# Kernel optimization log

Hardware: AMD Instinct MI355X
Metric: run time of the kernel (lower is better)

## Reference

```python
import jax, jax.numpy as jnp
import numpy as np

D_MODEL = 256
N_HEADS = 8
N_LEVELS = 4
NUM_POINTS_LIST = [4, 4, 4, 4]
SUM_POINTS = sum(NUM_POINTS_LIST)
TOTAL_POINTS = N_HEADS * SUM_POINTS
HEAD_DIM = D_MODEL // N_HEADS
OFFSET_SCALE = 0.5
SPATIAL_SHAPES = np.array([[80, 80], [40, 40], [20, 20], [10, 10]], dtype=np.int64)


def setup_inputs() -> dict:
    key = jax.random.key(0)
    ks = jax.random.split(key, 7)
    B, NQ = 16, 300
    seq = int((SPATIAL_SHAPES[:, 0] * SPATIAL_SHAPES[:, 1]).sum())  # 8500
    s = 1.0 / np.sqrt(D_MODEL)
    return {
        'hidden_states': jax.random.normal(ks[0], (B, NQ, D_MODEL), jnp.float32),
        'encoder_hidden_states': jax.random.normal(ks[1], (B, seq, D_MODEL), jnp.float32),
        'reference_points': jax.random.uniform(ks[2], (B, NQ, 1, 4), jnp.float32, 0.05, 0.95),
        'spatial_shapes': SPATIAL_SHAPES,
        'w_off': jax.random.uniform(ks[3], (TOTAL_POINTS * 2, D_MODEL), jnp.float32, -s, s),
        'b_off': jax.random.uniform(ks[4], (TOTAL_POINTS * 2,), jnp.float32, -s, s),
        'w_attn': jax.random.uniform(ks[5], (TOTAL_POINTS, D_MODEL), jnp.float32, -s, s),
        'b_attn': jax.random.uniform(ks[6], (TOTAL_POINTS,), jnp.float32, -s, s),
    }


def _grid_sample_zeros(img_flat, H, W, gx, gy):
    # img_flat: [N, H*W, C]; gx, gy: [N, Q, P] unnormalized pixel coords.
    # Bilinear, padding_mode='zeros', align_corners=False semantics of torch.grid_sample.
    x0 = jnp.floor(gx)
    y0 = jnp.floor(gy)
    wx = (gx - x0)[..., None]
    wy = (gy - y0)[..., None]
    x0i = x0.astype(jnp.int32)
    y0i = y0.astype(jnp.int32)

    def gather(xi, yi):
        valid = (xi >= 0) & (xi < W) & (yi >= 0) & (yi < H)
        idx = jnp.clip(yi, 0, H - 1) * W + jnp.clip(xi, 0, W - 1)
        N = img_flat.shape[0]
        v = jnp.take_along_axis(img_flat, idx.reshape(N, -1)[..., None], axis=1)
        v = v.reshape(idx.shape + (img_flat.shape[-1],))
        return v * valid[..., None]

    v00 = gather(x0i, y0i)
    v01 = gather(x0i + 1, y0i)
    v10 = gather(x0i, y0i + 1)
    v11 = gather(x0i + 1, y0i + 1)
    top = v00 * (1 - wx) + v01 * wx
    bot = v10 * (1 - wx) + v11 * wx
    return top * (1 - wy) + bot * wy  # [N, Q, P, C]


def reference(hidden_states, encoder_hidden_states, reference_points, spatial_shapes, w_off, b_off, w_attn, b_attn):
    B, NQ, _ = hidden_states.shape
    seq = encoder_hidden_states.shape[1]
    shapes = np.asarray(spatial_shapes)

    value = encoder_hidden_states.reshape(B, seq, N_HEADS, HEAD_DIM)

    off = (hidden_states @ w_off.T + b_off).reshape(B, NQ, N_HEADS, SUM_POINTS, 2)
    attn = jax.nn.softmax((hidden_states @ w_attn.T + b_attn).reshape(B, NQ, N_HEADS, SUM_POINTS), axis=-1)

    # reference_points: [B, NQ, 1, 4] (cx, cy, w, h) in [0,1]
    nps = jnp.asarray(np.repeat([1.0 / n for n in NUM_POINTS_LIST], NUM_POINTS_LIST), hidden_states.dtype)[:, None]
    offset = off * nps * reference_points[:, :, None, :, 2:] * OFFSET_SCALE
    sampling_locations = reference_points[:, :, None, :, :2] + offset  # [B,NQ,H,P,2]

    grids = 2.0 * sampling_locations - 1.0
    value_bh = value.transpose(0, 2, 1, 3).reshape(B * N_HEADS, seq, HEAD_DIM)
    grids_bh = grids.transpose(0, 2, 1, 3, 4).reshape(B * N_HEADS, NQ, SUM_POINTS, 2)

    outs = []
    start_s, start_p = 0, 0
    for lvl in range(N_LEVELS):
        Hl, Wl = int(shapes[lvl, 0]), int(shapes[lvl, 1])
        Pl = NUM_POINTS_LIST[lvl]
        img = value_bh[:, start_s:start_s + Hl * Wl]  # [BH, Hl*Wl, hd]
        g = grids_bh[:, :, start_p:start_p + Pl]
        gx = (g[..., 0] + 1.0) * Wl / 2.0 - 0.5
        gy = (g[..., 1] + 1.0) * Hl / 2.0 - 0.5
        outs.append(_grid_sample_zeros(img, Hl, Wl, gx, gy))
        start_s += Hl * Wl
        start_p += Pl

    sampled = jnp.concatenate(outs, axis=2)  # [BH, NQ, SUM_POINTS, hd]
    attn_bh = attn.transpose(0, 2, 1, 3).reshape(B * N_HEADS, NQ, SUM_POINTS, 1)
    out = (sampled * attn_bh).sum(axis=2)  # [BH, NQ, hd]
    out = out.reshape(B, N_HEADS, NQ, HEAD_DIM).transpose(0, 2, 1, 3).reshape(B, NQ, D_MODEL)
    return (out, attn)
```

## Files before the change

kernel.cpp:

```cpp
#include <hip/hip_runtime.h>
#include <hip/hip_bf16.h>

#define BQ_TOTAL 4800
#define D_MODEL 256
#define N_HEADS 8
#define SUM_POINTS 16
#define HEAD_DIM 32
#define SEQ 8500
#define OUT_ELEMS (BQ_TOTAL * D_MODEL)

typedef _Float16 half8 __attribute__((ext_vector_type(8)));
typedef _Float16 half4 __attribute__((ext_vector_type(4)));
typedef float floatx4 __attribute__((ext_vector_type(4)));

#define LDK 264

__global__ __launch_bounds__(256) void gemm_logits_mfma(
    const float* __restrict__ hs,
    const float* __restrict__ w_off, const float* __restrict__ b_off,
    const float* __restrict__ w_attn, const float* __restrict__ b_attn,
    float* __restrict__ off_out, float* __restrict__ attn_out)
{
    __shared__ _Float16 Asld[64 * LDK];
    __shared__ _Float16 Bsld[64 * LDK];

    const int tid = threadIdx.x;
    const int row0 = blockIdx.x * 64;
    const int col0 = blockIdx.y * 64;

    const float* Bsrc; const float* bias;
    if (col0 < 256) { Bsrc = w_off  + (size_t)col0 * 256;        bias = b_off  + col0; }
    else            { Bsrc = w_attn + (size_t)(col0 - 256) * 256; bias = b_attn + (col0 - 256); }

    #pragma unroll
    for (int i = 0; i < 16; i++) {
        const int idx = tid + i * 256;
        const int r = idx >> 6;
        const int kc = (idx & 63) << 2;

        const float4 a = *(const float4*)(hs + (size_t)(row0 + r) * 256 + kc);
        half4 ah; ah[0] = (_Float16)a.x; ah[1] = (_Float16)a.y;
                  ah[2] = (_Float16)a.z; ah[3] = (_Float16)a.w;
        *(half4*)&Asld[r * LDK + kc] = ah;

        const float4 b = *(const float4*)(Bsrc + (size_t)r * 256 + kc);
        half4 bh; bh[0] = (_Float16)b.x; bh[1] = (_Float16)b.y;
                  bh[2] = (_Float16)b.z; bh[3] = (_Float16)b.w;
        *(half4*)&Bsld[r * LDK + kc] = bh;
    }
    __syncthreads();

    const int wv = tid >> 6;
    const int lane = tid & 63;
    const int m = lane & 15;
    const int quad = lane >> 4;

    half8 af[8];
    #pragma unroll
    for (int q8 = 0; q8 < 8; q8++)
        af[q8] = *(const half8*)&Asld[(wv * 16 + m) * LDK + q8 * 32 + quad * 8];

    floatx4 acc[4] = {{0.f,0.f,0.f,0.f},{0.f,0.f,0.f,0.f},{0.f,0.f,0.f,0.f},{0.f,0.f,0.f,0.f}};
    #pragma unroll
    for (int ct = 0; ct < 4; ct++) {
        #pragma unroll
        for (int q8 = 0; q8 < 8; q8++) {
            const half8 bf = *(const half8*)&Bsld[(ct * 16 + m) * LDK + q8 * 32 + quad * 8];
            acc[ct] = __builtin_amdgcn_mfma_f32_16x16x32_f16(af[q8], bf, acc[ct], 0, 0, 0);
        }
    }

    #pragma unroll
    for (int ct = 0; ct < 4; ct++) {
        const int col_l = ct * 16 + m;
        const float bv = bias[col_l];
        #pragma unroll
        for (int rg = 0; rg < 4; rg++) {
            const int row = row0 + wv * 16 + quad * 4 + rg;
            const float v = acc[ct][rg] + bv;
            if (col0 < 256)
                off_out[(size_t)row * 256 + col0 + col_l] = v;
            else
                attn_out[(size_t)row * 128 + (col0 - 256) + col_l] = v;
        }
    }
}

__global__ __launch_bounds__(256) void deform_sample(
    const float* __restrict__ enc,
    const float* __restrict__ refp,
    const float* __restrict__ offlog,
    float* __restrict__ attn,
    float* __restrict__ out)
{
    const int tid = threadIdx.x;
    const int w = tid >> 6;
    const int lane = tid & 63;
    const int item = blockIdx.x * 4 + w;
    const int bq = item >> 3;
    const int h = item & 7;
    const int p = lane >> 2;
    const int sub = lane & 3;

    float* attn_ptr = attn + (size_t)bq * 128 + h * 16;
    const float l = attn_ptr[p];
    float m = l;
    #pragma unroll
    for (int s = 4; s < 64; s <<= 1) m = fmaxf(m, __shfl_xor(m, s));
    const float e = __expf(l - m);
    float ssum = e;
    #pragma unroll
    for (int s = 4; s < 64; s <<= 1) ssum += __shfl_xor(ssum, s);
    const float prob = e / ssum;
    if (sub == 0) attn_ptr[p] = prob;

    const float2 off2 = *(const float2*)(offlog + (size_t)bq * 256 + h * 32 + 2 * p);
    const float* rp = refp + (size_t)bq * 4;
    const float cx = rp[0], cy = rp[1], rw = rp[2], rh = rp[3];

    const int lvl = p >> 2;
    const int Wl = 80 >> lvl;
    int base = 0;
    if (lvl == 1) base = 6400;
    else if (lvl == 2) base = 8000;
    else if (lvl == 3) base = 8400;

    const float Wf = (float)Wl;
    const float gx = (cx + off2.x * 0.125f * rw) * Wf - 0.5f;
    const float gy = (cy + off2.y * 0.125f * rh) * Wf - 0.5f;
    const float x0f = floorf(gx), y0f = floorf(gy);
    const float fx = gx - x0f, fy = gy - y0f;
    const int x0 = (int)x0f, y0 = (int)y0f;

    const int b = bq / 300;
    const float* pbase = enc + ((size_t)b * SEQ + base) * 256 + h * 32 + sub * 4;

    float4 acc0 = {0.f, 0.f, 0.f, 0.f};
    float4 acc1 = {0.f, 0.f, 0.f, 0.f};
    #pragma unroll
    for (int c = 0; c < 4; c++) {
        const int xc = x0 + (c & 1);
        const int yc = y0 + (c >> 1);
        const float wx = (c & 1) ? fx : (1.0f - fx);
        const float wy = (c >> 1) ? fy : (1.0f - fy);
        const bool valid = (xc >= 0) && (xc < Wl) && (yc >= 0) && (yc < Wl);
        const int xi = min(max(xc, 0), Wl - 1);
        const int yi = min(max(yc, 0), Wl - 1);
        const float wgt = valid ? wx * wy : 0.0f;
        const float* vp = pbase + (size_t)(yi * Wl + xi) * 256;
        const float4 va = *(const float4*)(vp);
        const float4 vb = *(const float4*)(vp + 16);
        acc0.x += wgt * va.x; acc0.y += wgt * va.y;
        acc0.z += wgt * va.z; acc0.w += wgt * va.w;
        acc1.x += wgt * vb.x; acc1.y += wgt * vb.y;
        acc1.z += wgt * vb.z; acc1.w += wgt * vb.w;
    }

    float vals[8];
    vals[0] = acc0.x * prob; vals[1] = acc0.y * prob;
    vals[2] = acc0.z * prob; vals[3] = acc0.w * prob;
    vals[4] = acc1.x * prob; vals[5] = acc1.y * prob;
    vals[6] = acc1.z * prob; vals[7] = acc1.w * prob;

    #pragma unroll
    for (int s = 4; s < 64; s <<= 1) {
        #pragma unroll
        for (int j = 0; j < 8; j++) vals[j] += __shfl_xor(vals[j], s);
    }

    if (lane < 8) {
        const int halfs = lane >> 2;
        const int sb = lane & 3;
        float4 v;
        if (halfs == 0) { v.x = vals[0]; v.y = vals[1]; v.z = vals[2]; v.w = vals[3]; }
        else            { v.x = vals[4]; v.y = vals[5]; v.z = vals[6]; v.w = vals[7]; }
        out[(size_t)bq * 256 + h * 32 + halfs * 16 + sb * 4 + 0] = v.x;
        out[(size_t)bq * 256 + h * 32 + halfs * 16 + sb * 4 + 1] = v.y;
        out[(size_t)bq * 256 + h * 32 + halfs * 16 + sb * 4 + 2] = v.z;
        out[(size_t)bq * 256 + h * 32 + halfs * 16 + sb * 4 + 3] = v.w;
    }
}

extern "C" void kernel_launch(void* const* d_in, const int* in_sizes, int n_in,
                              void* d_out, int out_size, void* d_ws, size_t ws_size,
                              hipStream_t stream) {
    const float* hs     = (const float*)d_in[0];
    const float* enc    = (const float*)d_in[1];
    const float* refp   = (const float*)d_in[2];
    const float* w_off  = (const float*)d_in[4];
    const float* b_off  = (const float*)d_in[5];
    const float* w_attn = (const float*)d_in[6];
    const float* b_attn = (const float*)d_in[7];

    float* out  = (float*)d_out;
    float* attn = out + OUT_ELEMS;
    float* offlog = (float*)d_ws;

    dim3 g1(BQ_TOTAL / 64, 384 / 64);
    gemm_logits_mfma<<<g1, 256, 0, stream>>>(hs, w_off, b_off, w_attn, b_attn, offlog, attn);

    deform_sample<<<(BQ_TOTAL * N_HEADS) / 4, 256, 0, stream>>>(enc, refp, offlog, attn, out);
}
```

Before: 216.3 us.

## Swizzle sampling blocks across XCDs, hoist loads, and halve shuffle reduction

Remaps block indices so each XCD's round-robin share covers a contiguous range of queries, aiming to keep the gathered encoder rows for one batch resident in a single L2. Offset and reference-point loads are issued before the softmax shuffles, and the reference point is read as one float4. The cross-point reduction first swaps halves of the 8 channel values between lane halves, cutting shuffle count, and the result is stored as a float4. The swizzle hard-codes the grid size and XCD count.

```diff
diff --git a/kernel.cpp b/kernel.cpp
--- a/kernel.cpp
+++ b/kernel.cpp
@@ -96,7 +96,11 @@
     const int tid = threadIdx.x;
     const int w = tid >> 6;
     const int lane = tid & 63;
-    const int item = blockIdx.x * 4 + w;
+
+    const int orig = blockIdx.x;
+    const int bswz = (orig & 7) * 1200 + (orig >> 3);
+
+    const int item = bswz * 4 + w;
     const int bq = item >> 3;
     const int h = item & 7;
     const int p = lane >> 2;
@@ -104,6 +108,9 @@
 
     float* attn_ptr = attn + (size_t)bq * 128 + h * 16;
     const float l = attn_ptr[p];
+    const float2 off2 = *(const float2*)(offlog + (size_t)bq * 256 + h * 32 + 2 * p);
+    const float4 rp4 = *(const float4*)(refp + (size_t)bq * 4);
+
     float m = l;
     #pragma unroll
     for (int s = 4; s < 64; s <<= 1) m = fmaxf(m, __shfl_xor(m, s));
@@ -114,9 +121,7 @@
     const float prob = e / ssum;
     if (sub == 0) attn_ptr[p] = prob;
 
-    const float2 off2 = *(const float2*)(offlog + (size_t)bq * 256 + h * 32 + 2 * p);
-    const float* rp = refp + (size_t)bq * 4;
-    const float cx = rp[0], cy = rp[1], rw = rp[2], rh = rp[3];
+    const float cx = rp4.x, cy = rp4.y, rw = rp4.z, rh = rp4.w;
 
     const int lvl = p >> 2;
     const int Wl = 80 >> lvl;
@@ -162,22 +167,22 @@
     vals[4] = acc1.x * prob; vals[5] = acc1.y * prob;
     vals[6] = acc1.z * prob; vals[7] = acc1.w * prob;
 
-    #pragma unroll
-    for (int s = 4; s < 64; s <<= 1) {
+    float red[4];
+    #pragma unroll
+    for (int i = 0; i < 4; i++) {
+        const float send = (lane & 32) ? vals[i] : vals[i + 4];
+        const float recv = __shfl_xor(send, 32);
+        red[i] = ((lane & 32) ? vals[i + 4] : vals[i]) + recv;
+    }
+    #pragma unroll
+    for (int s = 4; s < 32; s <<= 1) {
         #pragma unroll
-        for (int j = 0; j < 8; j++) vals[j] += __shfl_xor(vals[j], s);
-    }
-
-    if (lane < 8) {
-        const int halfs = lane >> 2;
-        const int sb = lane & 3;
-        float4 v;
-        if (halfs == 0) { v.x = vals[0]; v.y = vals[1]; v.z = vals[2]; v.w = vals[3]; }
-        else            { v.x = vals[4]; v.y = vals[5]; v.z = vals[6]; v.w = vals[7]; }
-        out[(size_t)bq * 256 + h * 32 + halfs * 16 + sb * 4 + 0] = v.x;
-        out[(size_t)bq * 256 + h * 32 + halfs * 16 + sb * 4 + 1] = v.y;
-        out[(size_t)bq * 256 + h * 32 + halfs * 16 + sb * 4 + 2] = v.z;
-        out[(size_t)bq * 256 + h * 32 + halfs * 16 + sb * 4 + 3] = v.w;
+        for (int i = 0; i < 4; i++) red[i] += __shfl_xor(red[i], s);
+    }
+
+    if ((lane & 28) == 0) {
+        float4 v; v.x = red[0]; v.y = red[1]; v.z = red[2]; v.w = red[3];
+        *(float4*)(out + (size_t)bq * 256 + h * 32 + ((lane >> 5) << 4) + (sub << 2)) = v;
     }
 }
 
```

After: 219.4 us. No clear change (+1.4%).
